# Kernel optimization log

Measured on AMD Instinct MI355X. Metric: run time of the kernel, lower is better.

Reference implementation:

```python
import jax, jax.numpy as jnp
import numpy as np

B, F, Q, E = 256, 128, 4096, 128
TAU = 0.2
P_DROP = 0.5
NUM_SAMPLES = 128  # hardcoded in forward: compute_scores(..., num_samples=128)
NUM_POS = 1
EASY_UB = 0.5
HARD_LB = 0.5


def setup_inputs() -> dict:
    k = jax.random.key(0)
    ks = jax.random.split(k, 8)
    query = jax.random.normal(ks[0], (B, F), jnp.float32)
    key = jax.random.normal(ks[1], (B, F), jnp.float32)
    teacher = jax.random.normal(ks[2], (B, F), jnp.float32)
    negatives = jax.random.normal(ks[3], (F, Q), jnp.float32)
    # random_maskout masks: rand <= p -> zero out
    mask_t = jax.random.uniform(ks[4], (E, B, F)) <= P_DROP
    mask_n = jax.random.uniform(ks[5], (E, F, Q)) <= P_DROP
    # compute_scores sampling mask: rand <= num_samples/Q
    score_mask = jax.random.uniform(ks[6], (E, B, Q)) <= (NUM_SAMPLES / Q)
    # bootstrap over batch dim: for each (e,q) column, sample B row indices with replacement
    idx = jax.random.randint(ks[7], (E, Q, B), 0, B)
    boot = jnp.zeros((E, Q, B), bool).at[
        jnp.arange(E)[:, None, None], jnp.arange(Q)[None, :, None], idx
    ].set(True)
    boot_mask = jnp.transpose(boot, (0, 2, 1))  # (E,B,Q)
    return dict(query=query, key=key, teacher=teacher, negatives=negatives,
                mask_t=mask_t, mask_n=mask_n, score_mask=score_mask, boot_mask=boot_mask)


def _masked_softmax(x, mask, axis):
    # matches torch masked_fill(~mask, -inf) + softmax; masked entries -> 0 prob
    z = jnp.where(mask, x, -jnp.inf)
    m = jnp.max(z, axis=axis, keepdims=True)
    m = jnp.where(jnp.isfinite(m), m, 0.0)  # guard fully-masked slices
    e = jnp.where(mask, jnp.exp(z - m), 0.0)
    return e / jnp.maximum(e.sum(axis=axis, keepdims=True), 1e-30)


def _l2norm(x, axis):
    n = jnp.sqrt(jnp.sum(x * x, axis=axis, keepdims=True))
    return x / jnp.maximum(n, 1e-12)


def reference(query, key, teacher, negatives, mask_t, mask_n, score_mask, boot_mask):
    negatives = jax.lax.stop_gradient(negatives)  # negatives.detach().clone()
    logits_pos = jnp.sum(query * key, axis=1, keepdims=True)      # (B,1)
    logits_neg = query @ negatives                                 # (B,Q)
    logits = jnp.concatenate([logits_pos, logits_neg], axis=1) / TAU
    moco_loss = -jax.nn.log_softmax(logits, axis=1)[:, 0].mean()   # CE with target 0

    # ---- teacher similarities (torch.no_grad) ----
    t = _l2norm(jnp.where(mask_t, 0.0, teacher[None, :, :]), 2)    # (E,B,F)
    n = _l2norm(jnp.where(mask_n, 0.0, negatives[None, :, :]), 1)  # (E,F,Q)
    sim = jax.lax.stop_gradient(jnp.einsum('ebf,efq->ebq', t, n) / TAU)

    # ---- scores: masked softmax over Q, masked mean over E ----
    probs = _masked_softmax(sim, score_mask, axis=2)               # (E,B,Q)
    cnt_e = jnp.maximum(score_mask.sum(axis=0).astype(sim.dtype), 1.0)
    scores = probs.sum(axis=0) / cnt_e                             # (B,Q)

    # ---- uncertainty: masked entropy over batch dim ----
    p = _masked_softmax(sim, boot_mask, axis=1) + 1e-7             # (E,B,Q)
    ent = -(p * jnp.log(p))
    cnt_b = jnp.maximum(boot_mask.sum(axis=1).astype(sim.dtype), 1.0)  # (E,Q)
    uncertainty = (ent.sum(axis=1) / cnt_b).mean(axis=0, keepdims=True)  # (1,Q)

    log_sm_neg = jax.nn.log_softmax(logits[:, 1:], axis=1)         # (B,Q)

    def _pos_loss(pos_mask_row):
        pm = jnp.broadcast_to(pos_mask_row, (B, Q))
        s = jnp.where(pm, scores, -jnp.inf)
        _, idx = jax.lax.top_k(s, NUM_POS)                         # (B,k)
        loss = -jnp.take_along_axis(log_sm_neg, idx, axis=1).mean(axis=1).mean()
        mask = jnp.zeros((B, Q), bool).at[jnp.arange(B)[:, None], idx].set(True)
        return loss, mask

    ub = jnp.quantile(uncertainty, EASY_UB, axis=1)                # (1,)
    easy_loss, easy_mask = _pos_loss(uncertainty <= ub)
    lb = jnp.quantile(uncertainty, HARD_LB, axis=1)
    hard_loss, hard_mask = _pos_loss(uncertainty >= lb)

    return moco_loss, logits, easy_loss, easy_mask, hard_loss, hard_mask
```

## Files before the change

### kernel.cpp

```cpp
#include <hip/hip_runtime.h>
#include <cmath>

typedef unsigned char u8;
typedef unsigned short u16;
typedef unsigned int u32;
typedef __attribute__((ext_vector_type(8))) short s8v;
typedef __attribute__((ext_vector_type(4))) float f32x4;

#define B 256
#define F 128
#define Q 4096
#define E 128
#define QW 128
#define INV_TAU 5.0f
#define CAP 256

#define W_SCORES 0u
#define W_CNT    1048576u
#define W_UNC    2097152u
#define W_NLSE   2101248u
#define W_MOCO   2101504u
#define W_EASY   2101760u
#define W_HARD   2102016u
#define W_UB     2102272u
#define W_INVN   2102528u
#define W_AF     2626816u
#define W_PB     4723968u
#define W_PS     8918272u
#define W_PN     13112576u
#define W_CNTB   15209728u
#define W_ENT    15242496u

#define O_MOCO   0u
#define O_LOGITS 1u
#define O_ELOSS  1048833u
#define O_EMASK  1048834u
#define O_HLOSS  2097410u
#define O_HMASK  2097411u

static __device__ __forceinline__ u16 f2bf(float x) {
    unsigned int u = __builtin_bit_cast(unsigned int, x);
    unsigned int r = (u + 0x7FFFu + ((u >> 16) & 1u)) >> 16;
    return (u16)r;
}

__global__ void k_zero(float4* __restrict__ p) {
    p[(size_t)blockIdx.x * 256 + threadIdx.x] = make_float4(0.f, 0.f, 0.f, 0.f);
}
__global__ void k_zeroi(int* __restrict__ p) {
    p[(size_t)blockIdx.x * 256 + threadIdx.x] = 0;
}

__global__ void __launch_bounds__(256) k_pack(const u8* __restrict__ in,
                                              u32* __restrict__ out, int Rin) {
    __shared__ u32 lds[64 * 133];
    int t = threadIdx.x;
    int r0 = blockIdx.x * 64;
    int q0 = blockIdx.y * 512;
    int qw0 = q0 >> 5;
    #pragma unroll
    for (int i = 0; i < 8; i++) {
        int w = i * 256 + t;
        int row = w >> 5, c = w & 31;
        uint4 v = *(const uint4*)&in[(size_t)(r0 + row) * Q + q0 + c * 16];
        int base = row * 133 + c * 4;
        lds[base] = v.x; lds[base + 1] = v.y; lds[base + 2] = v.z; lds[base + 3] = v.w;
    }
    __syncthreads();
    int e = r0 / Rin, rr = r0 % Rin;
    #pragma unroll
    for (int k = 0; k < 4; k++) {
        int qw = (t >> 6) + k * 4;
        int r = t & 63;
        u32 w = 0;
        #pragma unroll
        for (int j = 0; j < 8; j++) {
            u32 u = lds[r * 133 + qw * 8 + j];
            w |= ((u & 1u) | ((u >> 7) & 2u) | ((u >> 14) & 4u) | ((u >> 21) & 8u)) << (j * 4);
        }
        out[((size_t)e * QW + qw0 + qw) * Rin + rr + r] = w;
    }
}

__global__ void k_afrag(const float* __restrict__ teacher, const u8* __restrict__ mask_t,
                        u16* __restrict__ af) {
    int eb = blockIdx.x;
    int e  = eb >> 8;
    int b  = eb & (B - 1);
    int f  = threadIdx.x;
    float v = mask_t[(size_t)eb * F + f] ? 0.f : teacher[b * F + f];
    float ss = v * v;
    #pragma unroll
    for (int o = 32; o > 0; o >>= 1) ss += __shfl_down(ss, o);
    __shared__ float s2[2];
    if ((threadIdx.x & 63) == 0) s2[threadIdx.x >> 6] = ss;
    __syncthreads();
    float d = fmaxf(sqrtf(s2[0] + s2[1]), 1e-12f);
    float t = v / d;
    int bg = b >> 4, m = b & 15;
    int kb = f >> 5, quad = (f >> 3) & 3, j = f & 7;
    int lane = quad * 16 + m;
    af[((((size_t)e * 16 + bg) * 4 + kb) * 64 + lane) * 8 + j] = f2bf(t);
}

__global__ void __launch_bounds__(256) k_invn(const float* __restrict__ neg,
                                              const u32* __restrict__ pn,
                                              float* __restrict__ invn) {
    __shared__ u32 lds[32 * 128];
    int e = blockIdx.x, t = threadIdx.x;
    int qblk = blockIdx.y;
    size_t base = ((size_t)e * QW + qblk * 32) * F;
    #pragma unroll
    for (int k = 0; k < 16; k++) lds[t + 256 * k] = pn[base + t + 256 * k];
    __syncthreads();
    int q0 = qblk * 1024 + t * 4;
    int qwl = (t * 4) >> 5;
    int sh = (t * 4) & 31;
    float s0 = 0.f, s1 = 0.f, s2 = 0.f, s3 = 0.f;
    #pragma unroll 4
    for (int f = 0; f < F; f++) {
        float4 v = *(const float4*)&neg[(size_t)f * Q + q0];
        u32 w = lds[qwl * 128 + f] >> sh;
        if (!(w & 1u)) s0 = fmaf(v.x, v.x, s0);
        if (!(w & 2u)) s1 = fmaf(v.y, v.y, s1);
        if (!(w & 4u)) s2 = fmaf(v.z, v.z, s2);
        if (!(w & 8u)) s3 = fmaf(v.w, v.w, s3);
    }
    float4 r;
    r.x = INV_TAU / fmaxf(sqrtf(s0), 1e-12f);
    r.y = INV_TAU / fmaxf(sqrtf(s1), 1e-12f);
    r.z = INV_TAU / fmaxf(sqrtf(s2), 1e-12f);
    r.w = INV_TAU / fmaxf(sqrtf(s3), 1e-12f);
    *(float4*)&invn[(size_t)e * Q + q0] = r;
}

__global__ void __launch_bounds__(256) k_fused(
        const u16* __restrict__ af, const float* __restrict__ neg,
        const u32* __restrict__ pn, const float* __restrict__ invn,
        const u32* __restrict__ pb, const u32* __restrict__ ps,
        float* __restrict__ unc, uint2* __restrict__ ent_buf,
        int* __restrict__ cnt_buf, int e0) {
    __shared__ u16 bfrag[4][4][512];
    __shared__ u32 bw[2][256], sw[2][256];
    __shared__ u32 pnl[2][128];
    __shared__ float invl[64];
    __shared__ float sstat[4][64], cstat[4][64], estat[4][64];
    __shared__ float carr[64];
    __shared__ int sbase[256];

    int qb = blockIdx.x;
    int el = blockIdx.y, e = e0 + el;
    int t = threadIdx.x;
    int q0 = qb * 64;
    int qw0 = qb * 2;

    bw[0][t] = pb[((size_t)e * QW + qw0) * B + t];
    bw[1][t] = pb[((size_t)e * QW + qw0 + 1) * B + t];
    sw[0][t] = ps[((size_t)e * QW + qw0) * B + t];
    sw[1][t] = ps[((size_t)e * QW + qw0 + 1) * B + t];
    if (t < 128) {
        pnl[0][t] = pn[((size_t)e * QW + qw0) * F + t];
        pnl[1][t] = pn[((size_t)e * QW + qw0 + 1) * F + t];
    } else if (t < 192) {
        invl[t - 128] = invn[(size_t)e * Q + q0 + (t - 128)];
    }
    __syncthreads();

    #pragma unroll
    for (int s = 0; s < 4; s++) {
        int slot = t + 256 * s;
        int qg = slot >> 8;
        int r = slot & 255;
        int kb = r >> 6, lane2 = r & 63;
        int ql = qg * 16 + (lane2 & 15);
        int fb = kb * 32 + (lane2 >> 4) * 8;
        float iv = invl[ql];
        const u32* pw = pnl[ql >> 5];
        int sh = ql & 31;
        u16 tmp[8];
        #pragma unroll
        for (int j = 0; j < 8; j++) {
            u32 bit = (pw[fb + j] >> sh) & 1u;
            float v = bit ? 0.f : neg[(size_t)(fb + j) * Q + q0 + ql] * iv;
            tmp[j] = f2bf(v);
        }
        *(s8v*)&bfrag[qg][kb][lane2 * 8] = *(const s8v*)tmp;
    }
    __syncthreads();

    int wave = t >> 6, lane = t & 63;
    int colb = lane & 15, quad = lane >> 4;
    f32x4 acc[4][4];
    #pragma unroll
    for (int bgi = 0; bgi < 4; bgi++) {
        int bg = wave * 4 + bgi;
        s8v a[4];
        #pragma unroll
        for (int kb = 0; kb < 4; kb++)
            a[kb] = *(const s8v*)&af[((((size_t)e * 16 + bg) * 4 + kb) * 64 + lane) * 8];
        #pragma unroll
        for (int qg = 0; qg < 4; qg++) {
            f32x4 c4 = {0.f, 0.f, 0.f, 0.f};
            #pragma unroll
            for (int kb = 0; kb < 4; kb++) {
                s8v bv = *(const s8v*)&bfrag[qg][kb][lane * 8];
                c4 = __builtin_amdgcn_mfma_f32_16x16x32_bf16(a[kb], bv, c4, 0, 0, 0);
            }
            acc[bgi][qg] = c4;
        }
    }

    float sloc[4] = {0.f, 0.f, 0.f, 0.f}, cloc[4] = {0.f, 0.f, 0.f, 0.f};
    #pragma unroll
    for (int bgi = 0; bgi < 4; bgi++) {
        int b0 = (wave * 4 + bgi) * 16 + quad * 4;
        uint4 w0 = *(const uint4*)&bw[0][b0];
        uint4 w1 = *(const uint4*)&bw[1][b0];
        u32 W0[4] = {w0.x, w0.y, w0.z, w0.w};
        u32 W1[4] = {w1.x, w1.y, w1.z, w1.w};
        #pragma unroll
        for (int r = 0; r < 4; r++)
            #pragma unroll
            for (int qg = 0; qg < 4; qg++) {
                u32 w = (qg & 2) ? W1[r] : W0[r];
                int bpos = (qg & 1) * 16 + colb;
                if ((w >> bpos) & 1u) {
                    sloc[qg] += __expf(acc[bgi][qg][r]);
                    cloc[qg] += 1.f;
                }
            }
    }
    #pragma unroll
    for (int qg = 0; qg < 4; qg++) {
        sloc[qg] += __shfl_xor(sloc[qg], 16); sloc[qg] += __shfl_xor(sloc[qg], 32);
        cloc[qg] += __shfl_xor(cloc[qg], 16); cloc[qg] += __shfl_xor(cloc[qg], 32);
    }
    if (quad == 0)
        #pragma unroll
        for (int qg = 0; qg < 4; qg++) {
            sstat[wave][qg * 16 + colb] = sloc[qg];
            cstat[wave][qg * 16 + colb] = cloc[qg];
        }
    __syncthreads();
    float invS[4];
    #pragma unroll
    for (int qg = 0; qg < 4; qg++) {
        int c = qg * 16 + colb;
        float S = sstat[0][c] + sstat[1][c] + sstat[2][c] + sstat[3][c];
        invS[qg] = 1.f / fmaxf(S, 1e-30f);
    }
    if (wave == 0 && quad == 0)
        #pragma unroll
        for (int qg = 0; qg < 4; qg++) {
            int c = qg * 16 + colb;
            carr[c] = cstat[0][c] + cstat[1][c] + cstat[2][c] + cstat[3][c];
        }

    const float P0 = 1e-7f;
    const float C0 = 1.61180954e-6f;
    float eloc[4] = {0.f, 0.f, 0.f, 0.f};
    #pragma unroll
    for (int bgi = 0; bgi < 4; bgi++) {
        int b0 = (wave * 4 + bgi) * 16 + quad * 4;
        uint4 w0 = *(const uint4*)&bw[0][b0];
        uint4 w1 = *(const uint4*)&bw[1][b0];
        u32 W0[4] = {w0.x, w0.y, w0.z, w0.w};
        u32 W1[4] = {w1.x, w1.y, w1.z, w1.w};
        #pragma unroll
        for (int r = 0; r < 4; r++)
            #pragma unroll
            for (int qg = 0; qg < 4; qg++) {
                u32 w = (qg & 2) ? W1[r] : W0[r];
                int bpos = (qg & 1) * 16 + colb;
                if ((w >> bpos) & 1u) {
                    float p = __expf(acc[bgi][qg][r]) * invS[qg] + P0;
                    eloc[qg] -= p * __logf(p);
                } else {
                    eloc[qg] += C0;
                }
            }
    }
    #pragma unroll
    for (int qg = 0; qg < 4; qg++) {
        eloc[qg] += __shfl_xor(eloc[qg], 16); eloc[qg] += __shfl_xor(eloc[qg], 32);
    }
    if (quad == 0)
        #pragma unroll
        for (int qg = 0; qg < 4; qg++) estat[wave][qg * 16 + colb] = eloc[qg];

    {
        u32 a0 = sw[0][t], a1 = sw[1][t];
        int n = __popc(a0) + __popc(a1);
        int base = 0;
        if (n) base = atomicAdd(&cnt_buf[el * B + t], n);
        sbase[t] = base;
    }
    __syncthreads();

    if (t < 64) {
        float tot = estat[0][t] + estat[1][t] + estat[2][t] + estat[3][t];
        atomicAdd(&unc[q0 + t], tot / fmaxf(carr[t], 1.f));
    }

    #pragma unroll
    for (int bgi = 0; bgi < 4; bgi++) {
        int b0 = (wave * 4 + bgi) * 16 + quad * 4;
        uint4 s0 = *(const uint4*)&sw[0][b0];
        uint4 s1 = *(const uint4*)&sw[1][b0];
        u32 S0[4] = {s0.x, s0.y, s0.z, s0.w};
        u32 S1[4] = {s1.x, s1.y, s1.z, s1.w};
        #pragma unroll
        for (int r = 0; r < 4; r++) {
            int bs = sbase[b0 + r];
            int p0 = __popc(S0[r]);
            #pragma unroll
            for (int qg = 0; qg < 4; qg++) {
                int bpos = (qg & 1) * 16 + colb;
                u32 w = (qg & 2) ? S1[r] : S0[r];
                if ((w >> bpos) & 1u) {
                    int rank = __popc(w & ((1u << bpos) - 1u)) + ((qg & 2) ? p0 : 0);
                    int pos = bs + rank;
                    if (pos < CAP) {
                        uint2 en;
                        en.x = (unsigned)(q0 + qg * 16 + colb);
                        en.y = __builtin_bit_cast(unsigned, acc[bgi][qg][r]);
                        ent_buf[((size_t)(el * B + b0 + r)) * CAP + pos] = en;
                    }
                }
            }
        }
    }
}

__global__ void __launch_bounds__(256) k_scores(
        const uint2* __restrict__ ent_buf, const int* __restrict__ cnt_buf,
        float* __restrict__ sacc, float* __restrict__ cacc, int ecnt) {
    __shared__ float srow[Q];
    __shared__ float crow[Q];
    int b = blockIdx.x, t = threadIdx.x;
    #pragma unroll
    for (int j = 0; j < 16; j++) { srow[t + 256 * j] = 0.f; crow[t + 256 * j] = 0.f; }
    __syncthreads();
    int wave = t >> 6, lane = t & 63;
    for (int el = wave; el < ecnt; el += 4) {
        int c = cnt_buf[el * B + b];
        if (c > CAP) c = CAP;
        if (c == 0) continue;
        const uint2* p = ent_buf + (size_t)(el * B + b) * CAP;
        uint2 ev[4]; float exv[4]; int ne = 0;
        float s = 0.f;
        for (int i = lane; i < c; i += 64) {
            ev[ne] = p[i];
            exv[ne] = __expf(__builtin_bit_cast(float, ev[ne].y));
            s += exv[ne];
            ne++;
        }
        #pragma unroll
        for (int off = 32; off > 0; off >>= 1) s += __shfl_xor(s, off);
        float iS = 1.f / fmaxf(s, 1e-30f);
        for (int k = 0; k < ne; k++) {
            atomicAdd(&srow[ev[k].x], exv[k] * iS);
            atomicAdd(&crow[ev[k].x], 1.f);
        }
    }
    __syncthreads();
    #pragma unroll
    for (int j = 0; j < 16; j++) {
        int q = t + 256 * j;
        sacc[(size_t)b * Q + q] += srow[q];
        cacc[(size_t)b * Q + q] += crow[q];
    }
}

__global__ void k_finscores(float* __restrict__ sacc, const float* __restrict__ cacc) {
    int idx = blockIdx.x * 256 + threadIdx.x;
    sacc[idx] = sacc[idx] / fmaxf(cacc[idx], 1.f);
}

__global__ void k_logits(const float* __restrict__ query, const float* __restrict__ key,
                         const float* __restrict__ neg, float* __restrict__ out) {
    __shared__ float qrow[F];
    __shared__ float red[256];
    int b = blockIdx.x, seg = blockIdx.y, t = threadIdx.x;
    if (t < F) qrow[t] = query[b * F + t];
    __syncthreads();
    int q0 = seg * 1024 + t * 4;
    float4 acc = make_float4(0.f, 0.f, 0.f, 0.f);
    for (int f = 0; f < F; f++) {
        float a = qrow[f];
        float4 v = *(const float4*)&neg[(size_t)f * Q + q0];
        acc.x = fmaf(a, v.x, acc.x);
        acc.y = fmaf(a, v.y, acc.y);
        acc.z = fmaf(a, v.z, acc.z);
        acc.w = fmaf(a, v.w, acc.w);
    }
    float* row = out + O_LOGITS + (size_t)b * (Q + 1);
    row[1 + q0]     = acc.x * INV_TAU;
    row[1 + q0 + 1] = acc.y * INV_TAU;
    row[1 + q0 + 2] = acc.z * INV_TAU;
    row[1 + q0 + 3] = acc.w * INV_TAU;
    if (seg == 0) {
        float pp = (t < F) ? qrow[t] * key[b * F + t] : 0.f;
        red[t] = pp;
        __syncthreads();
        for (int s = 128; s > 0; s >>= 1) { if (t < s) red[t] += red[t + s]; __syncthreads(); }
        if (t == 0) row[0] = red[0] * INV_TAU;
    }
}

__global__ void k_rowstats(const float* __restrict__ out, float* __restrict__ moco_part,
                           float* __restrict__ nlse) {
    __shared__ float red[256];
    int b = blockIdx.x, t = threadIdx.x;
    const float* row = out + O_LOGITS + (size_t)b * (Q + 1);
    float m = -INFINITY, mn = -INFINITY;
    for (int j = 0; j < 17; j++) {
        int i = t + 256 * j;
        if (i < Q + 1) { float zz = row[i]; m = fmaxf(m, zz); if (i >= 1) mn = fmaxf(mn, zz); }
    }
    red[t] = m; __syncthreads();
    for (int s = 128; s > 0; s >>= 1) { if (t < s) red[t] = fmaxf(red[t], red[t + s]); __syncthreads(); }
    float M = red[0]; __syncthreads();
    red[t] = mn; __syncthreads();
    for (int s = 128; s > 0; s >>= 1) { if (t < s) red[t] = fmaxf(red[t], red[t + s]); __syncthreads(); }
    float Mn = red[0]; __syncthreads();
    float s1 = 0.f, s2 = 0.f;
    for (int j = 0; j < 17; j++) {
        int i = t + 256 * j;
        if (i < Q + 1) { float zz = row[i]; s1 += expf(zz - M); if (i >= 1) s2 += expf(zz - Mn); }
    }
    red[t] = s1; __syncthreads();
    for (int s = 128; s > 0; s >>= 1) { if (t < s) red[t] += red[t + s]; __syncthreads(); }
    float S = red[0]; __syncthreads();
    red[t] = s2; __syncthreads();
    for (int s = 128; s > 0; s >>= 1) { if (t < s) red[t] += red[t + s]; __syncthreads(); }
    float Sn = red[0];
    if (t == 0) { moco_part[b] = M + logf(S) - row[0]; nlse[b] = Mn + logf(Sn); }
}

__global__ void k_median(float* __restrict__ unc, float* __restrict__ ubp) {
    __shared__ float sd[4096];
    int t = threadIdx.x;
    #pragma unroll
    for (int j = 0; j < 4; j++) {
        int q = t + 1024 * j;
        float u = unc[q] * (1.f / 128.f);
        unc[q] = u; sd[q] = u;
    }
    __syncthreads();
    for (int k = 2; k <= 4096; k <<= 1) {
        for (int j = k >> 1; j > 0; j >>= 1) {
            #pragma unroll
            for (int base = 0; base < 4; base++) {
                int i = t + 1024 * base;
                int ixj = i ^ j;
                if (ixj > i) {
                    bool up = ((i & k) == 0);
                    float x = sd[i], y = sd[ixj];
                    if ((x > y) == up) { sd[i] = y; sd[ixj] = x; }
                }
            }
            __syncthreads();
        }
    }
    if (t == 0) { float a = sd[2047], b2 = sd[2048]; ubp[0] = a + 0.5f * (b2 - a); }
}

__global__ void k_select(float* __restrict__ out, const float* __restrict__ scores,
                         const float* __restrict__ unc, const float* __restrict__ ubp,
                         const float* __restrict__ nlse, float* __restrict__ easy_part,
                         float* __restrict__ hard_part) {
    __shared__ float rv[256];
    __shared__ int ri[256];
    __shared__ int bshare;
    int b = blockIdx.x, mode = blockIdx.y, t = threadIdx.x;
    float ub = ubp[0];
    float bv = -INFINITY; int bidx = Q;
    #pragma unroll
    for (int j = 0; j < 16; j++) {
        int q = t + 256 * j;
        float u = unc[q];
        bool ok = (mode == 0) ? (u <= ub) : (u >= ub);
        if (ok) {
            float v = scores[(size_t)b * Q + q];
            if (v > bv || (v == bv && q < bidx)) { bv = v; bidx = q; }
        }
    }
    rv[t] = bv; ri[t] = bidx; __syncthreads();
    for (int s = 128; s > 0; s >>= 1) {
        if (t < s) {
            float v2 = rv[t + s]; int i2 = ri[t + s];
            if (v2 > rv[t] || (v2 == rv[t] && i2 < ri[t])) { rv[t] = v2; ri[t] = i2; }
        }
        __syncthreads();
    }
    if (t == 0) {
        int best = ri[0]; bshare = best;
        float zz = out[O_LOGITS + (size_t)b * (Q + 1) + 1 + best];
        float loss = nlse[b] - zz;
        (mode == 0 ? easy_part : hard_part)[b] = loss;
    }
    __syncthreads();
    int best = bshare;
    float* mrow = out + (mode == 0 ? O_EMASK : O_HMASK) + (size_t)b * Q;
    #pragma unroll
    for (int j = 0; j < 16; j++) { int q = t + 256 * j; mrow[q] = (q == best) ? 1.f : 0.f; }
}

__global__ void k_scalars(const float* __restrict__ moco, const float* __restrict__ easyp,
                          const float* __restrict__ hardp, float* __restrict__ out) {
    __shared__ float red[256];
    int t = threadIdx.x;
    red[t] = moco[t]; __syncthreads();
    for (int s = 128; s > 0; s >>= 1) { if (t < s) red[t] += red[t + s]; __syncthreads(); }
    if (t == 0) out[O_MOCO] = red[0] / 256.f;
    __syncthreads();
    red[t] = easyp[t]; __syncthreads();
    for (int s = 128; s > 0; s >>= 1) { if (t < s) red[t] += red[t + s]; __syncthreads(); }
    if (t == 0) out[O_ELOSS] = red[0] / 256.f;
    __syncthreads();
    red[t] = hardp[t]; __syncthreads();
    for (int s = 128; s > 0; s >>= 1) { if (t < s) red[t] += red[t + s]; __syncthreads(); }
    if (t == 0) out[O_HLOSS] = red[0] / 256.f;
}

extern "C" void kernel_launch(void* const* d_in, const int* in_sizes, int n_in,
                              void* d_out, int out_size, void* d_ws, size_t ws_size,
                              hipStream_t stream) {
    const float* query   = (const float*)d_in[0];
    const float* key     = (const float*)d_in[1];
    const float* teacher = (const float*)d_in[2];
    const float* neg     = (const float*)d_in[3];
    const u8* mask_t     = (const u8*)d_in[4];
    const u8* mask_n     = (const u8*)d_in[5];
    const u8* score_mask = (const u8*)d_in[6];
    const u8* boot_mask  = (const u8*)d_in[7];
    float* out = (float*)d_out;
    float* ws  = (float*)d_ws;

    long ws_floats = (long)(ws_size / 4);
    int Ec = (int)((ws_floats - (long)W_ENT) / (long)(B * CAP * 2));
    if (Ec > E) Ec = E;
    if (Ec < 1) Ec = 1;

    u16* af = (u16*)(ws + W_AF);
    u32* pb = (u32*)(ws + W_PB);
    u32* ps = (u32*)(ws + W_PS);
    u32* pn = (u32*)(ws + W_PN);
    int* cnt_buf = (int*)(ws + W_CNTB);
    uint2* ent_buf = (uint2*)(ws + W_ENT);

    k_zero<<<2052, 256, 0, stream>>>((float4*)(ws + W_SCORES));
    k_pack<<<dim3((E * B) / 64, Q / 512), 256, 0, stream>>>(boot_mask, pb, B);
    k_pack<<<dim3((E * B) / 64, Q / 512), 256, 0, stream>>>(score_mask, ps, B);
    k_pack<<<dim3((E * F) / 64, Q / 512), 256, 0, stream>>>(mask_n, pn, F);
    k_afrag<<<E * B, 128, 0, stream>>>(teacher, mask_t, af);
    k_invn<<<dim3(E, 4), 256, 0, stream>>>(neg, pn, ws + W_INVN);
    k_logits<<<dim3(B, 4), 256, 0, stream>>>(query, key, neg, out);
    k_rowstats<<<B, 256, 0, stream>>>(out, ws + W_MOCO, ws + W_NLSE);

    for (int e0 = 0; e0 < E; e0 += Ec) {
        int ecnt = (E - e0 < Ec) ? (E - e0) : Ec;
        k_zeroi<<<ecnt, 256, 0, stream>>>(cnt_buf);
        k_fused<<<dim3(Q / 64, ecnt), 256, 0, stream>>>(
            af, neg, pn, ws + W_INVN, pb, ps, ws + W_UNC, ent_buf, cnt_buf, e0);
        k_scores<<<B, 256, 0, stream>>>(ent_buf, cnt_buf, ws + W_SCORES, ws + W_CNT, ecnt);
    }

    k_finscores<<<(B * Q) / 256, 256, 0, stream>>>(ws + W_SCORES, ws + W_CNT);
    k_median<<<1, 1024, 0, stream>>>(ws + W_UNC, ws + W_UB);
    k_select<<<dim3(B, 2), 256, 0, stream>>>(out, ws + W_SCORES, ws + W_UNC, ws + W_UB,
                                             ws + W_NLSE, ws + W_EASY, ws + W_HARD);
    k_scalars<<<1, 256, 0, stream>>>(ws + W_MOCO, ws + W_EASY, ws + W_HARD, out);
}
```

Before: 1.402 ms.

## Merge pack launches, fold finalize into select, precompute exp, widen scores kernel

Merges the three mask-pack launches into one 3D grid and moves the count buffer next to the scores so a single zero kernel clears both. The separate finalize-scores pass is dropped and the division happens inside the selection kernel. In the fused kernel, exp is computed once per accumulator element and stored in the entry buffer, so the entropy pass and the scores kernel no longer recompute it. It also skips rows with no sampled bits early, and the scores kernel runs 512 threads with per-chunk counts cached in LDS. These changes cut launch count, redundant transcendental work and memory passes. The cost is a heavier exp loop over every element, including masked ones.

```diff
diff --git a/kernel.cpp b/kernel.cpp
--- a/kernel.cpp
+++ b/kernel.cpp
@@ -18,18 +18,19 @@
 #define W_SCORES 0u
 #define W_CNT    1048576u
 #define W_UNC    2097152u
-#define W_NLSE   2101248u
-#define W_MOCO   2101504u
-#define W_EASY   2101760u
-#define W_HARD   2102016u
-#define W_UB     2102272u
-#define W_INVN   2102528u
-#define W_AF     2626816u
-#define W_PB     4723968u
-#define W_PS     8918272u
-#define W_PN     13112576u
-#define W_CNTB   15209728u
+#define W_CNTB   2101248u
+#define W_NLSE   2134016u
+#define W_MOCO   2134272u
+#define W_EASY   2134528u
+#define W_HARD   2134784u
+#define W_UB     2135040u
+#define W_INVN   2135296u
+#define W_AF     2659584u
+#define W_PB     4756736u
+#define W_PS     8951040u
+#define W_PN     13145344u
 #define W_ENT    15242496u
+#define NZERO    2134016u
 
 #define O_MOCO   0u
 #define O_LOGITS 1u
@@ -47,12 +48,17 @@
 __global__ void k_zero(float4* __restrict__ p) {
     p[(size_t)blockIdx.x * 256 + threadIdx.x] = make_float4(0.f, 0.f, 0.f, 0.f);
 }
-__global__ void k_zeroi(int* __restrict__ p) {
-    p[(size_t)blockIdx.x * 256 + threadIdx.x] = 0;
-}
-
-__global__ void __launch_bounds__(256) k_pack(const u8* __restrict__ in,
-                                              u32* __restrict__ out, int Rin) {
+
+__global__ void __launch_bounds__(256) k_pack(const u8* __restrict__ boot,
+                                              const u8* __restrict__ smask,
+                                              const u8* __restrict__ maskn,
+                                              u32* __restrict__ pb, u32* __restrict__ ps,
+                                              u32* __restrict__ pn) {
+    int z = blockIdx.z;
+    int Rin = (z == 2) ? F : B;
+    if (z == 2 && blockIdx.x >= 2048) return;
+    const u8* in = (z == 0) ? boot : (z == 1) ? smask : maskn;
+    u32* out = (z == 0) ? pb : (z == 1) ? ps : pn;
     __shared__ u32 lds[64 * 133];
     int t = threadIdx.x;
     int r0 = blockIdx.x * 64;
@@ -210,6 +216,14 @@
         }
     }
 
+    #pragma unroll
+    for (int bgi = 0; bgi < 4; bgi++)
+        #pragma unroll
+        for (int qg = 0; qg < 4; qg++)
+            #pragma unroll
+            for (int r = 0; r < 4; r++)
+                acc[bgi][qg][r] = __expf(acc[bgi][qg][r]);
+
     float sloc[4] = {0.f, 0.f, 0.f, 0.f}, cloc[4] = {0.f, 0.f, 0.f, 0.f};
     #pragma unroll
     for (int bgi = 0; bgi < 4; bgi++) {
@@ -225,7 +239,7 @@
                 u32 w = (qg & 2) ? W1[r] : W0[r];
                 int bpos = (qg & 1) * 16 + colb;
                 if ((w >> bpos) & 1u) {
-                    sloc[qg] += __expf(acc[bgi][qg][r]);
+                    sloc[qg] += acc[bgi][qg][r];
                     cloc[qg] += 1.f;
                 }
             }
@@ -273,7 +287,7 @@
                 u32 w = (qg & 2) ? W1[r] : W0[r];
                 int bpos = (qg & 1) * 16 + colb;
                 if ((w >> bpos) & 1u) {
-                    float p = __expf(acc[bgi][qg][r]) * invS[qg] + P0;
+                    float p = acc[bgi][qg][r] * invS[qg] + P0;
                     eloc[qg] -= p * __logf(p);
                 } else {
                     eloc[qg] += C0;
@@ -302,6 +316,7 @@
         atomicAdd(&unc[q0 + t], tot / fmaxf(carr[t], 1.f));
     }
 
+    u32 cmask = 0x00010001u << colb;
     #pragma unroll
     for (int bgi = 0; bgi < 4; bgi++) {
         int b0 = (wave * 4 + bgi) * 16 + quad * 4;
@@ -311,6 +326,7 @@
         u32 S1[4] = {s1.x, s1.y, s1.z, s1.w};
         #pragma unroll
         for (int r = 0; r < 4; r++) {
+            if (!((S0[r] | S1[r]) & cmask)) continue;
             int bs = sbase[b0 + r];
             int p0 = __popc(S0[r]);
             #pragma unroll
@@ -332,49 +348,47 @@
     }
 }
 
-__global__ void __launch_bounds__(256) k_scores(
+__global__ void __launch_bounds__(512) k_scores(
         const uint2* __restrict__ ent_buf, const int* __restrict__ cnt_buf,
         float* __restrict__ sacc, float* __restrict__ cacc, int ecnt) {
     __shared__ float srow[Q];
     __shared__ float crow[Q];
+    __shared__ int cl[E];
     int b = blockIdx.x, t = threadIdx.x;
     #pragma unroll
-    for (int j = 0; j < 16; j++) { srow[t + 256 * j] = 0.f; crow[t + 256 * j] = 0.f; }
+    for (int j = 0; j < 8; j++) { srow[t + 512 * j] = 0.f; crow[t + 512 * j] = 0.f; }
+    if (t < ecnt) {
+        int c = cnt_buf[t * B + b];
+        cl[t] = (c > CAP) ? CAP : c;
+    }
     __syncthreads();
     int wave = t >> 6, lane = t & 63;
-    for (int el = wave; el < ecnt; el += 4) {
-        int c = cnt_buf[el * B + b];
-        if (c > CAP) c = CAP;
+    for (int el = wave; el < ecnt; el += 8) {
+        int c = cl[el];
         if (c == 0) continue;
         const uint2* p = ent_buf + (size_t)(el * B + b) * CAP;
-        uint2 ev[4]; float exv[4]; int ne = 0;
+        uint2 ev[4]; int ne = 0;
         float s = 0.f;
         for (int i = lane; i < c; i += 64) {
             ev[ne] = p[i];
-            exv[ne] = __expf(__builtin_bit_cast(float, ev[ne].y));
-            s += exv[ne];
+            s += __builtin_bit_cast(float, ev[ne].y);
             ne++;
         }
         #pragma unroll
         for (int off = 32; off > 0; off >>= 1) s += __shfl_xor(s, off);
         float iS = 1.f / fmaxf(s, 1e-30f);
         for (int k = 0; k < ne; k++) {
-            atomicAdd(&srow[ev[k].x], exv[k] * iS);
+            atomicAdd(&srow[ev[k].x], __builtin_bit_cast(float, ev[k].y) * iS);
             atomicAdd(&crow[ev[k].x], 1.f);
         }
     }
     __syncthreads();
     #pragma unroll
-    for (int j = 0; j < 16; j++) {
-        int q = t + 256 * j;
+    for (int j = 0; j < 8; j++) {
+        int q = t + 512 * j;
         sacc[(size_t)b * Q + q] += srow[q];
         cacc[(size_t)b * Q + q] += crow[q];
     }
-}
-
-__global__ void k_finscores(float* __restrict__ sacc, const float* __restrict__ cacc) {
-    int idx = blockIdx.x * 256 + threadIdx.x;
-    sacc[idx] = sacc[idx] / fmaxf(cacc[idx], 1.f);
 }
 
 __global__ void k_logits(const float* __restrict__ query, const float* __restrict__ key,
@@ -466,7 +480,8 @@
     if (t == 0) { float a = sd[2047], b2 = sd[2048]; ubp[0] = a + 0.5f * (b2 - a); }
 }
 
-__global__ void k_select(float* __restrict__ out, const float* __restrict__ scores,
+__global__ void k_select(float* __restrict__ out, const float* __restrict__ sacc,
+                         const float* __restrict__ cacc,
                          const float* __restrict__ unc, const float* __restrict__ ubp,
                          const float* __restrict__ nlse, float* __restrict__ easy_part,
                          float* __restrict__ hard_part) {
@@ -482,7 +497,7 @@
         float u = unc[q];
         bool ok = (mode == 0) ? (u <= ub) : (u >= ub);
         if (ok) {
-            float v = scores[(size_t)b * Q + q];
+            float v = sacc[(size_t)b * Q + q] / fmaxf(cacc[(size_t)b * Q + q], 1.f);
             if (v > bv || (v == bv && q < bidx)) { bv = v; bidx = q; }
         }
     }
@@ -550,10 +565,9 @@
     int* cnt_buf = (int*)(ws + W_CNTB);
     uint2* ent_buf = (uint2*)(ws + W_ENT);
 
-    k_zero<<<2052, 256, 0, stream>>>((float4*)(ws + W_SCORES));
-    k_pack<<<dim3((E * B) / 64, Q / 512), 256, 0, stream>>>(boot_mask, pb, B);
-    k_pack<<<dim3((E * B) / 64, Q / 512), 256, 0, stream>>>(score_mask, ps, B);
-    k_pack<<<dim3((E * F) / 64, Q / 512), 256, 0, stream>>>(mask_n, pn, F);
+    k_zero<<<NZERO / 1024, 256, 0, stream>>>((float4*)(ws + W_SCORES));
+    k_pack<<<dim3((E * B) / 64, Q / 512, 3), 256, 0, stream>>>(
+        boot_mask, score_mask, mask_n, pb, ps, pn);
     k_afrag<<<E * B, 128, 0, stream>>>(teacher, mask_t, af);
     k_invn<<<dim3(E, 4), 256, 0, stream>>>(neg, pn, ws + W_INVN);
     k_logits<<<dim3(B, 4), 256, 0, stream>>>(query, key, neg, out);
@@ -561,15 +575,17 @@
 
     for (int e0 = 0; e0 < E; e0 += Ec) {
         int ecnt = (E - e0 < Ec) ? (E - e0) : Ec;
-        k_zeroi<<<ecnt, 256, 0, stream>>>(cnt_buf);
+        if (e0 > 0)
+            k_zero<<<32, 256, 0, stream>>>((float4*)(ws + W_CNTB));
         k_fused<<<dim3(Q / 64, ecnt), 256, 0, stream>>>(
             af, neg, pn, ws + W_INVN, pb, ps, ws + W_UNC, ent_buf, cnt_buf, e0);
-        k_scores<<<B, 256, 0, stream>>>(ent_buf, cnt_buf, ws + W_SCORES, ws + W_CNT, ecnt);
-    }
-
-    k_finscores<<<(B * Q) / 256, 256, 0, stream>>>(ws + W_SCORES, ws + W_CNT);
+        k_scores<<<B, 512, 0, stream>>>(ent_buf, cnt_buf,
+                                        ws + W_SCORES, ws + W_CNT, ecnt);
+    }
+
     k_median<<<1, 1024, 0, stream>>>(ws + W_UNC, ws + W_UB);
-    k_select<<<dim3(B, 2), 256, 0, stream>>>(out, ws + W_SCORES, ws + W_UNC, ws + W_UB,
+    k_select<<<dim3(B, 2), 256, 0, stream>>>(out, ws + W_SCORES, ws + W_CNT,
+                                             ws + W_UNC, ws + W_UB,
                                              ws + W_NLSE, ws + W_EASY, ws + W_HARD);
     k_scalars<<<1, 256, 0, stream>>>(ws + W_MOCO, ws + W_EASY, ws + W_HARD, out);
 }
```

Measured after the change: 1.477 ms. 1.05x slower.
